# Performance work log

Hardware: AMD Instinct MI355X
Metric: run time of the kernel (lower is better)

The kernel has to match this reference:

```python
import jax, jax.numpy as jnp
import numpy as np

NUM_HEADS = 16
HEAD_SIZE = 64
CTXT_LEN = 2048
N_EMBED = 1024
BATCH = 2


def setup_inputs() -> dict:
    key = jax.random.key(0)
    ks = jax.random.split(key, 5)
    s = 0.02  # realistic init scale for weights
    return {
        "x": jax.random.normal(ks[0], (BATCH, CTXT_LEN, N_EMBED), dtype=jnp.float32),
        "Wk": jax.random.normal(ks[1], (N_EMBED, NUM_HEADS * HEAD_SIZE), dtype=jnp.float32) * s,
        "bk": jnp.zeros((NUM_HEADS * HEAD_SIZE,), dtype=jnp.float32),
        "Wq": jax.random.normal(ks[2], (N_EMBED, NUM_HEADS * HEAD_SIZE), dtype=jnp.float32) * s,
        "bq": jnp.zeros((NUM_HEADS * HEAD_SIZE,), dtype=jnp.float32),
        "Wv": jax.random.normal(ks[3], (N_EMBED, NUM_HEADS * HEAD_SIZE), dtype=jnp.float32) * s,
        "bv": jnp.zeros((NUM_HEADS * HEAD_SIZE,), dtype=jnp.float32),
        "Wo": jax.random.normal(ks[4], (NUM_HEADS * HEAD_SIZE, N_EMBED), dtype=jnp.float32) * s,
        "bo": jnp.zeros((N_EMBED,), dtype=jnp.float32),
    }


def reference(x, Wk, bk, Wq, bq, Wv, bv, Wo, bo):
    B, T, E = x.shape
    H, D = NUM_HEADS, HEAD_SIZE
    # QKV projections -> [B, T, H, D]
    k = (x @ Wk + bk).reshape(B, T, H, D)
    q = (x @ Wq + bq).reshape(B, T, H, D)
    v = (x @ Wv + bv).reshape(B, T, H, D)
    # NOTE: source scales by 1/sqrt(n_embed), not 1/sqrt(head_size)
    scale = 1.0 / (E ** 0.5)
    wei = jnp.einsum('bthd,bshd->bhts', q, k) * scale  # [B, H, T, T]
    causal = jnp.tril(jnp.ones((T, T), dtype=bool))
    wei = jnp.where(causal, wei, -jnp.inf)
    wei = jax.nn.softmax(wei, axis=-1)
    # dropout p=0.0 -> identity
    out = jnp.einsum('bhts,bshd->bthd', wei, v).reshape(B, T, H * D)
    return out @ Wo + bo
```

## Files before the change

kernel.cpp:

```cpp
#include <hip/hip_runtime.h>

#define NH 16
#define HS 64
#define T_CTX 2048
#define NE 1024
#define NB 2
#define BT (NB*T_CTX)
#define HD (NH*HS)

typedef unsigned short u16;
typedef __bf16 bf16_t;
typedef bf16_t bf16x8 __attribute__((ext_vector_type(8)));
typedef float f32x4 __attribute__((ext_vector_type(4)));
typedef u16 u16x8 __attribute__((ext_vector_type(8)));
typedef u16 u16x4 __attribute__((ext_vector_type(4)));

#define GLDS(gp, lp) __builtin_amdgcn_global_load_lds( \
    (const __attribute__((address_space(1))) void*)(gp), \
    (__attribute__((address_space(3))) void*)(lp), 16, 0, 0)

__device__ __forceinline__ u16 f2bf(float f) {
  union { float f; unsigned u; } x; x.f = f;
  return (u16)((x.u + 0x7fffu + ((x.u >> 16) & 1u)) >> 16);
}
__device__ __forceinline__ float bf2f(u16 u) {
  union { unsigned u; float f; } x; x.u = ((unsigned)u) << 16;
  return x.f;
}
__device__ __forceinline__ unsigned pack_bf2(float hi, float lo) {
  union { float f; unsigned u; } H, L; H.f = hi; L.f = lo;
  return __builtin_amdgcn_perm(H.u + 0x8000u, L.u + 0x8000u, 0x07060302);
}

__global__ __launch_bounds__(256) void k_prep_x(const float* __restrict__ x,
                                                u16* __restrict__ xb) {
  int i = blockIdx.x * blockDim.x + threadIdx.x;
  float4 v = ((const float4*)x)[i];
  ushort4 o;
  o.x = f2bf(v.x); o.y = f2bf(v.y); o.z = f2bf(v.z); o.w = f2bf(v.w);
  ((ushort4*)xb)[i] = o;
}

__global__ __launch_bounds__(256) void k_prep_w(
    const float* __restrict__ W0, const float* __restrict__ W1,
    const float* __restrict__ W2, const float* __restrict__ W3,
    u16* __restrict__ T0, u16* __restrict__ T1,
    u16* __restrict__ T2, u16* __restrict__ T3) {
  const float* W; u16* T;
  switch (blockIdx.z) {
    case 0: W = W0; T = T0; break;
    case 1: W = W1; T = T1; break;
    case 2: W = W2; T = T2; break;
    default: W = W3; T = T3; break;
  }
  __shared__ u16 tile[64 * 72];
  int k0 = blockIdx.x * 64, n0 = blockIdx.y * 64;
  int tid = threadIdx.x;
#pragma unroll
  for (int it = 0; it < 4; ++it) {
    int ci = tid + it * 256;
    int k = ci >> 4, c = ci & 15;
    float4 v = *(const float4*)&W[(size_t)(k0 + k) * NE + n0 + c * 4];
    int n = c * 4;
    tile[(n + 0) * 72 + k] = f2bf(v.x);
    tile[(n + 1) * 72 + k] = f2bf(v.y);
    tile[(n + 2) * 72 + k] = f2bf(v.z);
    tile[(n + 3) * 72 + k] = f2bf(v.w);
  }
  __syncthreads();
#pragma unroll
  for (int it = 0; it < 2; ++it) {
    int co = tid + it * 256;
    int n = co >> 3, c = co & 7;
    u16x8 v = *(const u16x8*)&tile[n * 72 + c * 8];
    *(u16x8*)&T[(size_t)(n0 + n) * NE + k0 + c * 8] = v;
  }
}

__global__ __launch_bounds__(512, 2) void k_gemm_qkv(
    const u16* __restrict__ xb, const u16* __restrict__ Wt,
    const float* __restrict__ bq, const float* __restrict__ bk,
    const float* __restrict__ bv, u16* __restrict__ Qw,
    u16* __restrict__ Kw, u16* __restrict__ Vtw) {
  __shared__ u16 sh[65536];
  const int b = blockIdx.x;
  const int xcd = b & 7, ii = b >> 3;
  const int mt = xcd * 2 + (ii & 1);
  const int nt = ii >> 1;
  const int m0g = mt * 256;
  const size_t n0g = (size_t)nt * 256;

  const int tid = threadIdx.x, lane = tid & 63, w = tid >> 6;
  const int wr = w >> 2, wc = w & 3;
  const int l16 = lane & 15, q = lane >> 4;

  auto stageA = [&](int tt, int h) {
    u16* dst = sh + (h * 2 + (tt & 1)) * 8192;
    const u16* src = xb + (size_t)(m0g + h * 128) * NE + tt * 64;
#pragma unroll
    for (int s2 = 0; s2 < 2; ++s2) {
      int ci = tid + s2 * 512;
      int row = ci >> 3, c = ci & 7;
      int cs = c ^ (row & 7);
      GLDS(src + (size_t)row * NE + cs * 8, dst + ci * 8);
    }
  };
  auto stageB = [&](int tt, int h) {
    u16* dst = sh + 32768 + (h * 2 + (tt & 1)) * 8192;
    const u16* src = Wt + (n0g + h * 128) * NE + tt * 64;
#pragma unroll
    for (int s2 = 0; s2 < 2; ++s2) {
      int ci = tid + s2 * 512;
      int row = ci >> 3, c = ci & 7;
      int cs = c ^ (row & 7);
      GLDS(src + (size_t)row * NE + cs * 8, dst + ci * 8);
    }
  };
  auto ldA = [&](int p, int i, int s) {
    int r = i * 16 + l16;
    return *(const bf16x8*)&sh[(wr * 2 + p) * 8192 + r * 64 +
                               ((s * 4 + q) ^ (r & 7)) * 8];
  };
  auto ldB = [&](int p, int j, int s) {
    int r = (wc & 1) * 64 + j * 16 + l16;
    return *(const bf16x8*)&sh[32768 + ((wc >> 1) * 2 + p) * 8192 + r * 64 +
                               ((s * 4 + q) ^ (r & 7)) * 8];
  };

  f32x4 acc[8][4];
#pragma unroll
  for (int i = 0; i < 8; ++i)
#pragma unroll
    for (int j = 0; j < 4; ++j)
#pragma unroll
      for (int r = 0; r < 4; ++r) acc[i][j][r] = 0.f;

  stageA(0, 0); stageA(0, 1); stageB(0, 0); stageB(0, 1);
  stageA(1, 0); stageA(1, 1); stageB(1, 0); stageB(1, 1);
  asm volatile("s_waitcnt vmcnt(8)\n\ts_barrier" ::: "memory");

  bf16x8 a[4][2], bfr[4][2];
#pragma unroll 1
  for (int t = 0; t < 16; ++t) {
    const int p = t & 1;
#pragma unroll
    for (int i = 0; i < 4; ++i) { a[i][0] = ldA(p, i, 0); a[i][1] = ldA(p, i, 1); }
#pragma unroll
    for (int j = 0; j < 4; ++j) { bfr[j][0] = ldB(p, j, 0); bfr[j][1] = ldB(p, j, 1); }
    asm volatile("s_barrier" ::: "memory");
    __builtin_amdgcn_s_setprio(1);
#pragma unroll
    for (int s = 0; s < 2; ++s)
#pragma unroll
      for (int i = 0; i < 4; ++i)
#pragma unroll
        for (int j = 0; j < 2; ++j)
          acc[i][j] = __builtin_amdgcn_mfma_f32_16x16x32_bf16(a[i][s], bfr[j][s], acc[i][j], 0, 0, 0);
    __builtin_amdgcn_s_setprio(0);
    asm volatile("s_barrier" ::: "memory");
    if (t + 2 < 16) stageB(t + 2, 0);
    asm volatile("s_barrier" ::: "memory");
    __builtin_amdgcn_s_setprio(1);
#pragma unroll
    for (int s = 0; s < 2; ++s)
#pragma unroll
      for (int i = 0; i < 4; ++i)
#pragma unroll
        for (int j = 0; j < 2; ++j)
          acc[i][j + 2] = __builtin_amdgcn_mfma_f32_16x16x32_bf16(a[i][s], bfr[j + 2][s], acc[i][j + 2], 0, 0, 0);
    __builtin_amdgcn_s_setprio(0);
    asm volatile("s_barrier" ::: "memory");
#pragma unroll
    for (int i = 0; i < 4; ++i) { a[i][0] = ldA(p, i + 4, 0); a[i][1] = ldA(p, i + 4, 1); }
    if (t + 2 < 16) stageB(t + 2, 1);
    asm volatile("s_barrier" ::: "memory");
    __builtin_amdgcn_s_setprio(1);
#pragma unroll
    for (int s = 0; s < 2; ++s)
#pragma unroll
      for (int i = 0; i < 4; ++i)
#pragma unroll
        for (int j = 0; j < 2; ++j)
          acc[i + 4][j] = __builtin_amdgcn_mfma_f32_16x16x32_bf16(a[i][s], bfr[j][s], acc[i + 4][j], 0, 0, 0);
    __builtin_amdgcn_s_setprio(0);
    asm volatile("s_barrier" ::: "memory");
    if (t + 2 < 16) { stageA(t + 2, 0); stageA(t + 2, 1); }
    asm volatile("s_barrier" ::: "memory");
    __builtin_amdgcn_s_setprio(1);
#pragma unroll
    for (int s = 0; s < 2; ++s)
#pragma unroll
      for (int i = 0; i < 4; ++i)
#pragma unroll
        for (int j = 0; j < 2; ++j)
          acc[i + 4][j + 2] = __builtin_amdgcn_mfma_f32_16x16x32_bf16(a[i][s], bfr[j + 2][s], acc[i + 4][j + 2], 0, 0, 0);
    __builtin_amdgcn_s_setprio(0);
    if (t + 2 < 16)
      asm volatile("s_waitcnt vmcnt(8)\n\ts_barrier" ::: "memory");
    else if (t + 1 < 16)
      asm volatile("s_waitcnt vmcnt(0)\n\ts_barrier" ::: "memory");
    else
      asm volatile("s_barrier" ::: "memory");
  }

  u16* Es = sh;
  const int z = nt >> 2;
  const int n0z = (nt & 3) * 256;
  const int bb = m0g >> 11;
  if (z <= 1) {
    const float* bias = (z == 0) ? bq : bk;
    const float scale = (z == 0) ? 0.03125f * 1.4426950408889634f : 1.0f;
    u16* dst = (z == 0) ? Qw : Kw;
#pragma unroll 1
    for (int ph = 0; ph < 2; ++ph) {
      __syncthreads();
      if (wr == ph) {
#pragma unroll
        for (int j = 0; j < 4; ++j) {
          int n = wc * 64 + j * 16 + l16;
          float bn = bias[n0z + n];
#pragma unroll
          for (int i = 0; i < 8; ++i)
#pragma unroll
            for (int r = 0; r < 4; ++r) {
              int m = i * 16 + q * 4 + r;
              Es[m * 264 + n] = f2bf((acc[i][j][r] + bn) * scale);
            }
        }
      }
      __syncthreads();
#pragma unroll
      for (int it = 0; it < 8; ++it) {
        int idx = it * 512 + tid;
        int tl = idx >> 5, c = idx & 31;
        u16x8 v = *(const u16x8*)&Es[tl * 264 + c * 8];
        int ng = n0z + c * 8, h = ng >> 6, d = ng & 63;
        int mg = m0g + ph * 128 + tl;
        int tt2 = mg & (T_CTX - 1);
        *(u16x8*)&dst[(((size_t)(bb * NH + h)) * T_CTX + tt2) * HS + d] = v;
      }
    }
  } else {
#pragma unroll 1
    for (int ph = 0; ph < 2; ++ph) {
      __syncthreads();
      if (wr == ph) {
#pragma unroll
        for (int j = 0; j < 4; ++j) {
          int n = wc * 64 + j * 16 + l16;
          float bn = bv[n0z + n];
#pragma unroll
          for (int i = 0; i < 8; ++i) {
            int m = i * 16 + q * 4;
            u16x4 pk;
#pragma unroll
            for (int r = 0; r < 4; ++r) pk[r] = f2bf(acc[i][j][r] + bn);
            *(u16x4*)&Es[n * 136 + m] = pk;
          }
        }
      }
      __syncthreads();
#pragma unroll
      for (int it = 0; it < 8; ++it) {
        int idx = it * 512 + tid;
        int dl = idx >> 4, c = idx & 15;
        u16x8 v = *(const u16x8*)&Es[dl * 136 + c * 8];
        int ng = n0z + dl, h = ng >> 6, d = ng & 63;
        int tt2 = (m0g & (T_CTX - 1)) + ph * 128 + c * 8;
        *(u16x8*)&Vtw[(((size_t)(bb * NH + h)) * HS + d) * T_CTX + tt2] = v;
      }
    }
  }
}

__device__ __forceinline__ void stage_kv(const u16* __restrict__ Kp,
                                         const u16* __restrict__ Vp,
                                         int k0, u16* KsB, u16* VsB, int tid) {
#pragma unroll
  for (int it = 0; it < 2; ++it) {
    int ci = tid + it * 256;
    int row = ci >> 3, cc = ci & 7;
    int prow = (row & 32) | ((row & 12) << 1) | ((row & 16) >> 2) | (row & 3);
    int sw = (cc ^ (row & 7)) * 8;
    GLDS(Kp + (size_t)(k0 + prow) * HS + sw, KsB + ci * 8);
    GLDS(Vp + (size_t)row * T_CTX + k0 + sw, VsB + ci * 8);
  }
}

__global__ __launch_bounds__(256) void k_attn(
    const u16* __restrict__ Qw, const u16* __restrict__ Kw,
    const u16* __restrict__ Vtw, u16* __restrict__ op0,
    u16* __restrict__ op1, u16* __restrict__ op2,
    float* __restrict__ lsum) {
  __shared__ u16 Ks[3 * 64 * 64];
  __shared__ u16 Vs[3 * 64 * 64];

  const int b = blockIdx.x;
  const int xcd = b & 7, ii = b >> 3;
  const int bh = xcd + 8 * (ii & 3);
  const int x = ii >> 2;
  const int qt = 15 - x / 3;
  const int part = x - (15 - qt) * 3;
  const int ntiles = 2 * (qt + 1);
  const int npt = (ntiles + 2) / 3;
  const int klo = part * npt;
  const int khi = min(klo + npt, ntiles);
  const int qbase = qt * 128;

  const u16* Qp = Qw + (size_t)bh * T_CTX * HS;
  const u16* Kp = Kw + (size_t)bh * T_CTX * HS;
  const u16* Vp = Vtw + (size_t)bh * HS * T_CTX;

  const int tid = threadIdx.x, lane = tid & 63, w = tid >> 6;
  const int q = lane >> 4, c = lane & 15;
  const int rbase = w * 32;

  bf16x8 aq[2][2];
#pragma unroll
  for (int i = 0; i < 2; ++i)
#pragma unroll
    for (int s = 0; s < 2; ++s)
      aq[i][s] = *(const bf16x8*)&Qp[(size_t)(qbase + rbase + i * 16 + c) * HS + s * 32 + q * 8];

  f32x4 o[2][4];
  float lrow[2] = {0.f, 0.f};
#pragma unroll
  for (int i = 0; i < 2; ++i)
#pragma unroll
    for (int j = 0; j < 4; ++j)
#pragma unroll
      for (int r = 0; r < 4; ++r) o[i][j][r] = 0.f;

  if (klo < khi)     stage_kv(Kp, Vp, klo * 64,       Ks,        Vs,        tid);
  if (klo + 1 < khi) stage_kv(Kp, Vp, (klo + 1) * 64, Ks + 4096, Vs + 4096, tid);

  for (int kt = klo; kt < khi; ++kt) {
    const int k0 = kt * 64;
    const int idx = kt - klo;
    u16* KsB = Ks + (idx % 3) * 4096;
    u16* VsB = Vs + (idx % 3) * 4096;
    if (kt + 1 < khi) {
      asm volatile("s_waitcnt vmcnt(4)\n\ts_barrier" ::: "memory");
    } else {
      asm volatile("s_waitcnt vmcnt(0)\n\ts_barrier" ::: "memory");
    }
    if (kt + 2 < khi)
      stage_kv(Kp, Vp, (kt + 2) * 64,
               Ks + ((idx + 2) % 3) * 4096, Vs + ((idx + 2) % 3) * 4096, tid);

    f32x4 s[4][2];
#pragma unroll
    for (int i2 = 0; i2 < 4; ++i2) {
      int krow = i2 * 16 + c;
      bf16x8 kf0 = *(const bf16x8*)&KsB[krow * 64 + ((0 + q) ^ (krow & 7)) * 8];
      bf16x8 kf1 = *(const bf16x8*)&KsB[krow * 64 + ((4 + q) ^ (krow & 7)) * 8];
#pragma unroll
      for (int j2 = 0; j2 < 2; ++j2) {
        f32x4 z4 = {0.f, 0.f, 0.f, 0.f};
        z4 = __builtin_amdgcn_mfma_f32_16x16x32_bf16(kf0, aq[j2][0], z4, 0, 0, 0);
        s[i2][j2] = __builtin_amdgcn_mfma_f32_16x16x32_bf16(kf1, aq[j2][1], z4, 0, 0, 0);
      }
    }

    if (k0 + 63 > qbase + rbase) {
#pragma unroll
      for (int i2 = 0; i2 < 4; ++i2)
#pragma unroll
        for (int j2 = 0; j2 < 2; ++j2)
#pragma unroll
          for (int r = 0; r < 4; ++r) {
            int key = k0 + ((i2 >> 1) << 5) + (q << 3) + ((i2 & 1) << 2) + r;
            int qrow = qbase + rbase + j2 * 16 + c;
            if (key > qrow) s[i2][j2][r] = -1e30f;
          }
    }

#pragma unroll
    for (int i2 = 0; i2 < 4; ++i2)
#pragma unroll
      for (int j2 = 0; j2 < 2; ++j2)
#pragma unroll
        for (int r = 0; r < 4; ++r) {
          float p = __builtin_amdgcn_exp2f(s[i2][j2][r]);
          s[i2][j2][r] = p;
          lrow[j2] += p;
        }

#pragma unroll
    for (int ks = 0; ks < 2; ++ks) {
      bf16x8 bv4[4];
#pragma unroll
      for (int j = 0; j < 4; ++j) {
        int d = j * 16 + c;
        bv4[j] = *(const bf16x8*)&VsB[d * 64 + ((ks * 4 + q) ^ (d & 7)) * 8];
      }
#pragma unroll
      for (int i = 0; i < 2; ++i) {
        union { uint4 u; bf16x8 b; } af;
        af.u.x = pack_bf2(s[2 * ks][i][1],     s[2 * ks][i][0]);
        af.u.y = pack_bf2(s[2 * ks][i][3],     s[2 * ks][i][2]);
        af.u.z = pack_bf2(s[2 * ks + 1][i][1], s[2 * ks + 1][i][0]);
        af.u.w = pack_bf2(s[2 * ks + 1][i][3], s[2 * ks + 1][i][2]);
#pragma unroll
        for (int j = 0; j < 4; ++j)
          o[i][j] = __builtin_amdgcn_mfma_f32_16x16x32_bf16(af.b, bv4[j], o[i][j], 0, 0, 0);
      }
    }
  }

  u16* op = (part == 0) ? op0 : (part == 1 ? op1 : op2);
  const size_t row0 = (size_t)bh * T_CTX + qbase;
#pragma unroll
  for (int i = 0; i < 2; ++i) {
    lrow[i] += __shfl_xor(lrow[i], 16, 64);
    lrow[i] += __shfl_xor(lrow[i], 32, 64);
  }
  if (q == 0) {
#pragma unroll
    for (int i = 0; i < 2; ++i)
      lsum[(size_t)part * 65536 + row0 + rbase + i * 16 + c] = lrow[i];
  }
#pragma unroll
  for (int i = 0; i < 2; ++i)
#pragma unroll
    for (int r = 0; r < 4; ++r) {
      size_t t = row0 + rbase + i * 16 + q * 4 + r;
#pragma unroll
      for (int j = 0; j < 4; ++j)
        op[t * 64 + j * 16 + c] = f2bf(o[i][j][r]);
    }
}

__global__ __launch_bounds__(256) void k_combine(
    const u16* __restrict__ op0, const u16* __restrict__ op1,
    const u16* __restrict__ op2, const float* __restrict__ lsum,
    u16* __restrict__ att) {
  int idx = blockIdx.x * 256 + threadIdx.x;
  int row = idx >> 3, oct = idx & 7;
  float l0 = lsum[row], l1 = lsum[65536 + row], l2 = lsum[131072 + row];
  float inv = 1.f / (l0 + l1 + l2);
  u16x8 a = *(const u16x8*)&op0[(size_t)row * 64 + oct * 8];
  u16x8 b = *(const u16x8*)&op1[(size_t)row * 64 + oct * 8];
  u16x8 d = *(const u16x8*)&op2[(size_t)row * 64 + oct * 8];
  u16x8 ov;
#pragma unroll
  for (int e = 0; e < 8; ++e)
    ov[e] = f2bf((bf2f(a[e]) + bf2f(b[e]) + bf2f(d[e])) * inv);
  int bh = row >> 11, t = row & 2047, bb = bh >> 4, h = bh & 15;
  *(u16x8*)&att[((size_t)(bb * T_CTX + t)) * HD + h * 64 + oct * 8] = ov;
}

__global__ __launch_bounds__(256) void k_gemm_out(
    const u16* __restrict__ attb, const u16* __restrict__ Wot,
    const float* __restrict__ bo, float* __restrict__ out) {
  __shared__ u16 sh[3 * 6144];
  const int bx = blockIdx.x;
  const int xcd = bx & 7, ii = bx >> 3;
  const int m0 = (xcd + 8 * (ii & 7)) * 64;
  const int n0 = (ii >> 3) * 128;
  const int tid = threadIdx.x, lane = tid & 63, w = tid >> 6;
  const int wm = (w & 1) * 32, wn = (w >> 1) * 64;
  const int q = lane >> 4, l16 = lane & 15;
  const int qsw = q ^ ((l16 >> 1) & 3);

  auto stage = [&](int k0, int b) {
    u16* As = sh + b * 6144;
    u16* Bs = As + 2048;
    {
      int row = tid >> 2, cc = tid & 3;
      int cs = cc ^ ((row >> 1) & 3);
      GLDS(attb + (size_t)(m0 + row) * NE + k0 + cs * 8, As + (size_t)tid * 8);
    }
#pragma unroll
    for (int s2 = 0; s2 < 2; ++s2) {
      int ci = tid + s2 * 256;
      int row = ci >> 2, cc = ci & 3;
      int cs = cc ^ ((row >> 1) & 3);
      GLDS(Wot + (size_t)(n0 + row) * NE + k0 + cs * 8, Bs + (size_t)ci * 8);
    }
  };

  f32x4 acc[2][4];
#pragma unroll
  for (int i = 0; i < 2; ++i)
#pragma unroll
    for (int j = 0; j < 4; ++j)
#pragma unroll
      for (int r = 0; r < 4; ++r) acc[i][j][r] = 0.f;

  stage(0, 0);
  stage(32, 1);
  for (int kt = 0; kt < 32; ++kt) {
    u16* As = sh + (kt % 3) * 6144;
    u16* Bs = As + 2048;
    if (kt + 1 < 32)
      asm volatile("s_waitcnt vmcnt(3)\n\ts_barrier" ::: "memory");
    else
      asm volatile("s_waitcnt vmcnt(0)\n\ts_barrier" ::: "memory");
    if (kt + 2 < 32) stage((kt + 2) * 32, (kt + 2) % 3);
    bf16x8 av[2], bv4[4];
#pragma unroll
    for (int i = 0; i < 2; ++i) av[i]  = *(const bf16x8*)&As[(wm + i * 16 + l16) * 32 + qsw * 8];
#pragma unroll
    for (int j = 0; j < 4; ++j) bv4[j] = *(const bf16x8*)&Bs[(wn + j * 16 + l16) * 32 + qsw * 8];
#pragma unroll
    for (int i = 0; i < 2; ++i)
#pragma unroll
      for (int j = 0; j < 4; ++j)
        acc[i][j] = __builtin_amdgcn_mfma_f32_16x16x32_bf16(av[i], bv4[j], acc[i][j], 0, 0, 0);
  }
#pragma unroll
  for (int j = 0; j < 4; ++j) {
    int n = n0 + wn + j * 16 + l16;
    float bn = bo[n];
#pragma unroll
    for (int i = 0; i < 2; ++i)
#pragma unroll
      for (int r = 0; r < 4; ++r) {
        int m = m0 + wm + i * 16 + q * 4 + r;
        out[(size_t)m * NE + n] = acc[i][j][r] + bn;
      }
  }
}

extern "C" void kernel_launch(void* const* d_in, const int* in_sizes, int n_in,
                              void* d_out, int out_size, void* d_ws, size_t ws_size,
                              hipStream_t stream) {
  (void)in_sizes; (void)n_in; (void)out_size; (void)ws_size;
  const float* x  = (const float*)d_in[0];
  const float* Wk = (const float*)d_in[1];
  const float* bk = (const float*)d_in[2];
  const float* Wq = (const float*)d_in[3];
  const float* bq = (const float*)d_in[4];
  const float* Wv = (const float*)d_in[5];
  const float* bv = (const float*)d_in[6];
  const float* Wo = (const float*)d_in[7];
  const float* bo = (const float*)d_in[8];
  float* out = (float*)d_out;

  u16* base = (u16*)d_ws;
  const size_t M = 1024 * 1024;
  u16* xb   = base;
  u16* Wt   = base + 4 * M;
  u16* Wot  = base + 7 * M;
  u16* Qw   = base + 8 * M;
  u16* Kw   = base + 12 * M;
  u16* Vtw  = base + 16 * M;
  u16* op0  = base + 20 * M;
  u16* op1  = base + 24 * M;
  u16* op2  = base;
  float* lsum = (float*)(base + 4 * M);
  u16* attw = base + 12 * M;

  k_prep_x<<<dim3(BT * NE / 4 / 256), 256, 0, stream>>>(x, xb);
  k_prep_w<<<dim3(16, 16, 4), 256, 0, stream>>>(
      Wq, Wk, Wv, Wo, Wt, Wt + (size_t)NE * HD, Wt + (size_t)2 * NE * HD, Wot);
  k_gemm_qkv<<<dim3(192), 512, 0, stream>>>(xb, Wt, bq, bk, bv, Qw, Kw, Vtw);
  k_attn<<<dim3(1536), 256, 0, stream>>>(Qw, Kw, Vtw, op0, op1, op2, lsum);
  k_combine<<<dim3(2048), 256, 0, stream>>>(op0, op1, op2, lsum, attw);
  k_gemm_out<<<dim3(512), 256, 0, stream>>>(attw, Wot, bo, out);
}
```

Before: 184.6 us.

## Drop split-K attention partitioning and normalize output directly in attention kernel

Each attention block now processes the full causal key range for its query tile instead of one third of it. Normalization by the row sum then happens in-kernel, writing straight to the interleaved attention layout. This removes the combine kernel, its partial-output and row-sum traffic, and one launch. In exchange the grid shrinks from 1536 to 512 blocks with unbalanced per-block work, which may hurt occupancy and load balance on a GPU with many CUs.

```diff
diff --git a/kernel.cpp b/kernel.cpp
--- a/kernel.cpp
+++ b/kernel.cpp
@@ -289,22 +289,15 @@
 
 __global__ __launch_bounds__(256) void k_attn(
     const u16* __restrict__ Qw, const u16* __restrict__ Kw,
-    const u16* __restrict__ Vtw, u16* __restrict__ op0,
-    u16* __restrict__ op1, u16* __restrict__ op2,
-    float* __restrict__ lsum) {
+    const u16* __restrict__ Vtw, u16* __restrict__ att) {
   __shared__ u16 Ks[3 * 64 * 64];
   __shared__ u16 Vs[3 * 64 * 64];
 
   const int b = blockIdx.x;
   const int xcd = b & 7, ii = b >> 3;
   const int bh = xcd + 8 * (ii & 3);
-  const int x = ii >> 2;
-  const int qt = 15 - x / 3;
-  const int part = x - (15 - qt) * 3;
-  const int ntiles = 2 * (qt + 1);
-  const int npt = (ntiles + 2) / 3;
-  const int klo = part * npt;
-  const int khi = min(klo + npt, ntiles);
+  const int qt = 15 - (ii >> 2);
+  const int khi = 2 * (qt + 1);
   const int qbase = qt * 128;
 
   const u16* Qp = Qw + (size_t)bh * T_CTX * HS;
@@ -331,14 +324,13 @@
 #pragma unroll
       for (int r = 0; r < 4; ++r) o[i][j][r] = 0.f;
 
-  if (klo < khi)     stage_kv(Kp, Vp, klo * 64,       Ks,        Vs,        tid);
-  if (klo + 1 < khi) stage_kv(Kp, Vp, (klo + 1) * 64, Ks + 4096, Vs + 4096, tid);
-
-  for (int kt = klo; kt < khi; ++kt) {
+  stage_kv(Kp, Vp, 0,  Ks,        Vs,        tid);
+  stage_kv(Kp, Vp, 64, Ks + 4096, Vs + 4096, tid);
+
+  for (int kt = 0; kt < khi; ++kt) {
     const int k0 = kt * 64;
-    const int idx = kt - klo;
-    u16* KsB = Ks + (idx % 3) * 4096;
-    u16* VsB = Vs + (idx % 3) * 4096;
+    u16* KsB = Ks + (kt % 3) * 4096;
+    u16* VsB = Vs + (kt % 3) * 4096;
     if (kt + 1 < khi) {
       asm volatile("s_waitcnt vmcnt(4)\n\ts_barrier" ::: "memory");
     } else {
@@ -346,7 +338,7 @@
     }
     if (kt + 2 < khi)
       stage_kv(Kp, Vp, (kt + 2) * 64,
-               Ks + ((idx + 2) % 3) * 4096, Vs + ((idx + 2) % 3) * 4096, tid);
+               Ks + ((kt + 2) % 3) * 4096, Vs + ((kt + 2) % 3) * 4096, tid);
 
     f32x4 s[4][2];
 #pragma unroll
@@ -408,46 +400,24 @@
     }
   }
 
-  u16* op = (part == 0) ? op0 : (part == 1 ? op1 : op2);
-  const size_t row0 = (size_t)bh * T_CTX + qbase;
 #pragma unroll
   for (int i = 0; i < 2; ++i) {
     lrow[i] += __shfl_xor(lrow[i], 16, 64);
     lrow[i] += __shfl_xor(lrow[i], 32, 64);
   }
-  if (q == 0) {
-#pragma unroll
-    for (int i = 0; i < 2; ++i)
-      lsum[(size_t)part * 65536 + row0 + rbase + i * 16 + c] = lrow[i];
-  }
+  const int bb = bh >> 4, h = bh & 15;
+  u16* dst = att + ((size_t)(bb * T_CTX) + qbase + rbase) * HD + h * 64;
 #pragma unroll
   for (int i = 0; i < 2; ++i)
 #pragma unroll
     for (int r = 0; r < 4; ++r) {
-      size_t t = row0 + rbase + i * 16 + q * 4 + r;
+      float lr = __shfl(lrow[i], q * 4 + r, 64);
+      float linv = __builtin_amdgcn_rcpf(lr);
+      size_t ro = (size_t)(i * 16 + q * 4 + r) * HD;
 #pragma unroll
       for (int j = 0; j < 4; ++j)
-        op[t * 64 + j * 16 + c] = f2bf(o[i][j][r]);
-    }
-}
-
-__global__ __launch_bounds__(256) void k_combine(
-    const u16* __restrict__ op0, const u16* __restrict__ op1,
-    const u16* __restrict__ op2, const float* __restrict__ lsum,
-    u16* __restrict__ att) {
-  int idx = blockIdx.x * 256 + threadIdx.x;
-  int row = idx >> 3, oct = idx & 7;
-  float l0 = lsum[row], l1 = lsum[65536 + row], l2 = lsum[131072 + row];
-  float inv = 1.f / (l0 + l1 + l2);
-  u16x8 a = *(const u16x8*)&op0[(size_t)row * 64 + oct * 8];
-  u16x8 b = *(const u16x8*)&op1[(size_t)row * 64 + oct * 8];
-  u16x8 d = *(const u16x8*)&op2[(size_t)row * 64 + oct * 8];
-  u16x8 ov;
-#pragma unroll
-  for (int e = 0; e < 8; ++e)
-    ov[e] = f2bf((bf2f(a[e]) + bf2f(b[e]) + bf2f(d[e])) * inv);
-  int bh = row >> 11, t = row & 2047, bb = bh >> 4, h = bh & 15;
-  *(u16x8*)&att[((size_t)(bb * T_CTX + t)) * HD + h * 64 + oct * 8] = ov;
+        dst[ro + j * 16 + c] = f2bf(o[i][j][r] * linv);
+    }
 }
 
 __global__ __launch_bounds__(256) void k_gemm_out(
@@ -546,17 +516,12 @@
   u16* Qw   = base + 8 * M;
   u16* Kw   = base + 12 * M;
   u16* Vtw  = base + 16 * M;
-  u16* op0  = base + 20 * M;
-  u16* op1  = base + 24 * M;
-  u16* op2  = base;
-  float* lsum = (float*)(base + 4 * M);
-  u16* attw = base + 12 * M;
+  u16* attw = base + 20 * M;
 
   k_prep_x<<<dim3(BT * NE / 4 / 256), 256, 0, stream>>>(x, xb);
   k_prep_w<<<dim3(16, 16, 4), 256, 0, stream>>>(
       Wq, Wk, Wv, Wo, Wt, Wt + (size_t)NE * HD, Wt + (size_t)2 * NE * HD, Wot);
   k_gemm_qkv<<<dim3(192), 512, 0, stream>>>(xb, Wt, bq, bk, bv, Qw, Kw, Vtw);
-  k_attn<<<dim3(1536), 256, 0, stream>>>(Qw, Kw, Vtw, op0, op1, op2, lsum);
-  k_combine<<<dim3(2048), 256, 0, stream>>>(op0, op1, op2, lsum, attw);
+  k_attn<<<dim3(512), 256, 0, stream>>>(Qw, Kw, Vtw, attw);
   k_gemm_out<<<dim3(512), 256, 0, stream>>>(attw, Wot, bo, out);
 }
```

Result: slower. 192.6 us (+4.3%).

## Fuse split-K attention combine into output GEMM A-load and merge prep kernels

Applied to the files above, without the earlier changes.

Removes the separate combine kernel. The output GEMM now loads the three partial attention outputs and their row sums directly, normalises them, and writes the bf16 A tile into shared memory through registers, with the pipeline and waitcnt/barrier schedule restructured around this. It also merges the x conversion and weight transpose prep kernels into a single launch. Together these drop one round trip of the attention tensor through global memory and two kernel launches. The cost is that each output block re-reads the partials redundantly across N tiles, and the A path moves from async global-to-LDS loads to register loads with manual vmcnt accounting.

```diff
diff --git a/kernel.cpp b/kernel.cpp
--- a/kernel.cpp
+++ b/kernel.cpp
@@ -32,30 +32,33 @@
   return __builtin_amdgcn_perm(H.u + 0x8000u, L.u + 0x8000u, 0x07060302);
 }
 
-__global__ __launch_bounds__(256) void k_prep_x(const float* __restrict__ x,
-                                                u16* __restrict__ xb) {
-  int i = blockIdx.x * blockDim.x + threadIdx.x;
-  float4 v = ((const float4*)x)[i];
-  ushort4 o;
-  o.x = f2bf(v.x); o.y = f2bf(v.y); o.z = f2bf(v.z); o.w = f2bf(v.w);
-  ((ushort4*)xb)[i] = o;
-}
-
-__global__ __launch_bounds__(256) void k_prep_w(
+__global__ __launch_bounds__(256) void k_prep(
+    const float* __restrict__ x,
     const float* __restrict__ W0, const float* __restrict__ W1,
     const float* __restrict__ W2, const float* __restrict__ W3,
+    u16* __restrict__ xb,
     u16* __restrict__ T0, u16* __restrict__ T1,
     u16* __restrict__ T2, u16* __restrict__ T3) {
+  __shared__ u16 tile[64 * 72];
+  const int b = blockIdx.x;
+  const int tid = threadIdx.x;
+  if (b >= 1024) {
+    int i = (b - 1024) * 256 + tid;
+    float4 v = ((const float4*)x)[i];
+    ushort4 o;
+    o.x = f2bf(v.x); o.y = f2bf(v.y); o.z = f2bf(v.z); o.w = f2bf(v.w);
+    ((ushort4*)xb)[i] = o;
+    return;
+  }
+  const int wz = b >> 8, rem = b & 255;
+  const int k0 = (rem & 15) * 64, n0 = (rem >> 4) * 64;
   const float* W; u16* T;
-  switch (blockIdx.z) {
+  switch (wz) {
     case 0: W = W0; T = T0; break;
     case 1: W = W1; T = T1; break;
     case 2: W = W2; T = T2; break;
     default: W = W3; T = T3; break;
   }
-  __shared__ u16 tile[64 * 72];
-  int k0 = blockIdx.x * 64, n0 = blockIdx.y * 64;
-  int tid = threadIdx.x;
 #pragma unroll
   for (int it = 0; it < 4; ++it) {
     int ci = tid + it * 256;
@@ -431,28 +434,11 @@
     }
 }
 
-__global__ __launch_bounds__(256) void k_combine(
+__global__ __launch_bounds__(256) void k_gemm_out(
     const u16* __restrict__ op0, const u16* __restrict__ op1,
     const u16* __restrict__ op2, const float* __restrict__ lsum,
-    u16* __restrict__ att) {
-  int idx = blockIdx.x * 256 + threadIdx.x;
-  int row = idx >> 3, oct = idx & 7;
-  float l0 = lsum[row], l1 = lsum[65536 + row], l2 = lsum[131072 + row];
-  float inv = 1.f / (l0 + l1 + l2);
-  u16x8 a = *(const u16x8*)&op0[(size_t)row * 64 + oct * 8];
-  u16x8 b = *(const u16x8*)&op1[(size_t)row * 64 + oct * 8];
-  u16x8 d = *(const u16x8*)&op2[(size_t)row * 64 + oct * 8];
-  u16x8 ov;
-#pragma unroll
-  for (int e = 0; e < 8; ++e)
-    ov[e] = f2bf((bf2f(a[e]) + bf2f(b[e]) + bf2f(d[e])) * inv);
-  int bh = row >> 11, t = row & 2047, bb = bh >> 4, h = bh & 15;
-  *(u16x8*)&att[((size_t)(bb * T_CTX + t)) * HD + h * 64 + oct * 8] = ov;
-}
-
-__global__ __launch_bounds__(256) void k_gemm_out(
-    const u16* __restrict__ attb, const u16* __restrict__ Wot,
-    const float* __restrict__ bo, float* __restrict__ out) {
+    const u16* __restrict__ Wot, const float* __restrict__ bo,
+    float* __restrict__ out) {
   __shared__ u16 sh[3 * 6144];
   const int bx = blockIdx.x;
   const int xcd = bx & 7, ii = bx >> 3;
@@ -463,14 +449,13 @@
   const int q = lane >> 4, l16 = lane & 15;
   const int qsw = q ^ ((l16 >> 1) & 3);
 
-  auto stage = [&](int k0, int b) {
-    u16* As = sh + b * 6144;
-    u16* Bs = As + 2048;
-    {
-      int row = tid >> 2, cc = tid & 3;
-      int cs = cc ^ ((row >> 1) & 3);
-      GLDS(attb + (size_t)(m0 + row) * NE + k0 + cs * 8, As + (size_t)tid * 8);
-    }
+  const int arow = tid >> 2, acc4 = tid & 3;
+  const int acs = acc4 ^ ((arow >> 1) & 3);
+  const int m = m0 + arow;
+  const int bb = m >> 11, t = m & 2047;
+
+  auto stageB = [&](int k0, int b) {
+    u16* Bs = sh + b * 6144 + 2048;
 #pragma unroll
     for (int s2 = 0; s2 < 2; ++s2) {
       int ci = tid + s2 * 256;
@@ -480,6 +465,25 @@
     }
   };
 
+  struct ASet { u16x8 a0, a1, a2; float l0, l1, l2; };
+  auto loadA = [&](int kt, ASet& S) {
+    int k = kt * 32 + acs * 8;
+    int h = k >> 6, d0 = k & 63;
+    size_t orow = ((size_t)(bb * 16 + h)) * 2048 + t;
+    S.a0 = *(const u16x8*)&op0[orow * 64 + d0];
+    S.a1 = *(const u16x8*)&op1[orow * 64 + d0];
+    S.a2 = *(const u16x8*)&op2[orow * 64 + d0];
+    S.l0 = lsum[orow]; S.l1 = lsum[65536 + orow]; S.l2 = lsum[131072 + orow];
+  };
+  auto writeA = [&](int b, const ASet& S) {
+    float inv = 1.f / (S.l0 + S.l1 + S.l2);
+    u16x8 ov;
+#pragma unroll
+    for (int e = 0; e < 8; ++e)
+      ov[e] = f2bf((bf2f(S.a0[e]) + bf2f(S.a1[e]) + bf2f(S.a2[e])) * inv);
+    *(u16x8*)&sh[b * 6144 + (size_t)tid * 8] = ov;
+  };
+
   f32x4 acc[2][4];
 #pragma unroll
   for (int i = 0; i < 2; ++i)
@@ -488,26 +492,36 @@
 #pragma unroll
       for (int r = 0; r < 4; ++r) acc[i][j][r] = 0.f;
 
-  stage(0, 0);
-  stage(32, 1);
+  ASet SA;
+  loadA(0, SA); stageB(0, 0);
+  asm volatile("s_waitcnt vmcnt(2)");
+  writeA(0, SA);
+  loadA(1, SA); stageB(32, 1);
+  asm volatile("s_waitcnt lgkmcnt(0) vmcnt(8)\n\ts_barrier" ::: "memory");
+
   for (int kt = 0; kt < 32; ++kt) {
     u16* As = sh + (kt % 3) * 6144;
     u16* Bs = As + 2048;
-    if (kt + 1 < 32)
-      asm volatile("s_waitcnt vmcnt(3)\n\ts_barrier" ::: "memory");
-    else
-      asm volatile("s_waitcnt vmcnt(0)\n\ts_barrier" ::: "memory");
-    if (kt + 2 < 32) stage((kt + 2) * 32, (kt + 2) % 3);
+    if (kt + 1 < 32) {
+      asm volatile("s_waitcnt vmcnt(2)");
+      writeA((kt + 1) % 3, SA);
+    }
     bf16x8 av[2], bv4[4];
 #pragma unroll
     for (int i = 0; i < 2; ++i) av[i]  = *(const bf16x8*)&As[(wm + i * 16 + l16) * 32 + qsw * 8];
 #pragma unroll
     for (int j = 0; j < 4; ++j) bv4[j] = *(const bf16x8*)&Bs[(wn + j * 16 + l16) * 32 + qsw * 8];
+    if (kt + 2 < 32) loadA(kt + 2, SA);
 #pragma unroll
     for (int i = 0; i < 2; ++i)
 #pragma unroll
       for (int j = 0; j < 4; ++j)
         acc[i][j] = __builtin_amdgcn_mfma_f32_16x16x32_bf16(av[i], bv4[j], acc[i][j], 0, 0, 0);
+    if (kt + 2 < 32) stageB((kt + 2) * 32, (kt + 2) % 3);
+    if (kt + 2 < 32)
+      asm volatile("s_waitcnt lgkmcnt(0) vmcnt(8)\n\ts_barrier" ::: "memory");
+    else if (kt + 1 < 32)
+      asm volatile("s_waitcnt lgkmcnt(0) vmcnt(0)\n\ts_barrier" ::: "memory");
   }
 #pragma unroll
   for (int j = 0; j < 4; ++j) {
@@ -517,8 +531,8 @@
     for (int i = 0; i < 2; ++i)
 #pragma unroll
       for (int r = 0; r < 4; ++r) {
-        int m = m0 + wm + i * 16 + q * 4 + r;
-        out[(size_t)m * NE + n] = acc[i][j][r] + bn;
+        int mm = m0 + wm + i * 16 + q * 4 + r;
+        out[(size_t)mm * NE + n] = acc[i][j][r] + bn;
       }
   }
 }
@@ -550,13 +564,11 @@
   u16* op1  = base + 24 * M;
   u16* op2  = base;
   float* lsum = (float*)(base + 4 * M);
-  u16* attw = base + 12 * M;
-
-  k_prep_x<<<dim3(BT * NE / 4 / 256), 256, 0, stream>>>(x, xb);
-  k_prep_w<<<dim3(16, 16, 4), 256, 0, stream>>>(
-      Wq, Wk, Wv, Wo, Wt, Wt + (size_t)NE * HD, Wt + (size_t)2 * NE * HD, Wot);
+
+  k_prep<<<dim3(5120), 256, 0, stream>>>(
+      x, Wq, Wk, Wv, Wo, xb,
+      Wt, Wt + (size_t)NE * HD, Wt + (size_t)2 * NE * HD, Wot);
   k_gemm_qkv<<<dim3(192), 512, 0, stream>>>(xb, Wt, bq, bk, bv, Qw, Kw, Vtw);
   k_attn<<<dim3(1536), 256, 0, stream>>>(Qw, Kw, Vtw, op0, op1, op2, lsum);
-  k_combine<<<dim3(2048), 256, 0, stream>>>(op0, op1, op2, lsum, attw);
-  k_gemm_out<<<dim3(512), 256, 0, stream>>>(attw, Wot, bo, out);
-}
+  k_gemm_out<<<dim3(512), 256, 0, stream>>>(op0, op1, op2, lsum, Wot, bo, out);
+}
```

New measurement: 185.4 us, median of 2. No clear change (+0.4%).
